# Kernel tuning notes

Hardware: AMD Instinct MI355X
Metric: run time of the kernel (lower is better)

Reference implementation:

```python
import jax, jax.numpy as jnp
import numpy as np

HEADS = 8
DIM_HEAD = 64
MAX_REL = 200  # max_rel_dist


def setup_inputs() -> dict:
    key = jax.random.key(0)
    ks = jax.random.split(key, 5)
    B, N, D = 4, 2048, 512
    x = jax.random.normal(ks[0], (B, N, D), dtype=jnp.float32)
    temporal_mask = jax.random.randint(ks[1], (N, N), 0, 2, dtype=jnp.int32)
    gamma = jnp.ones((D,), jnp.float32)
    beta = jnp.zeros((D,), jnp.float32)
    Wqkv = jax.random.normal(ks[2], (D, 3 * HEADS * DIM_HEAD), dtype=jnp.float32) * 0.02
    Wout = jax.random.normal(ks[3], (HEADS * DIM_HEAD, D), dtype=jnp.float32) * 0.02
    bout = jnp.zeros((D,), jnp.float32)
    rel_table = jax.random.normal(ks[4], (2 * MAX_REL - 1,), dtype=jnp.float32) * 0.02
    return {"x": x, "gamma": gamma, "beta": beta, "Wqkv": Wqkv, "Wout": Wout,
            "bout": bout, "rel_table": rel_table, "temporal_mask": temporal_mask}


def reference(x, gamma, beta, Wqkv, Wout, bout, rel_table, temporal_mask):
    B, N, D = x.shape
    scale = DIM_HEAD ** -0.5
    # LayerNorm
    mu = jnp.mean(x, axis=-1, keepdims=True)
    var = jnp.mean(jnp.square(x - mu), axis=-1, keepdims=True)
    xn = (x - mu) * jax.lax.rsqrt(var + 1e-5) * gamma + beta
    # QKV projection (no bias), split heads: b n (h d) -> b h n d
    qkv = xn @ Wqkv  # [B, N, 3*H*d]
    q, k, v = jnp.split(qkv, 3, axis=-1)
    split = lambda t: t.reshape(B, N, HEADS, DIM_HEAD).transpose(0, 2, 1, 3)
    q, k, v = split(q), split(k), split(v)
    # scores with learned relative-position bias
    dots = jnp.einsum('bhnd,bhmd->bhnm', q, k) * scale  # [B,H,N,N]
    idx = jnp.arange(N)
    rel = jnp.clip(idx[:, None] - idx[None, :], -(MAX_REL - 1), MAX_REL - 1) + MAX_REL - 1
    dots = dots + rel_table[rel][None, None, :, :]
    # temporal mask (0 -> -inf); large negative for grad safety
    dots = jnp.where(temporal_mask[None, None, :, :] == 0, jnp.float32(-1e9), dots)
    attn = jax.nn.softmax(dots, axis=-1)
    out = jnp.einsum('bhnm,bhmd->bhnd', attn, v)
    out = out.transpose(0, 2, 1, 3).reshape(B, N, HEADS * DIM_HEAD)
    return out @ Wout + bout
```

## Files before the change

### kernel.cpp

```cpp
#include <hip/hip_runtime.h>

typedef __attribute__((ext_vector_type(8))) short bf16x8;
typedef __attribute__((ext_vector_type(4))) short bf16x4;
typedef __attribute__((ext_vector_type(4))) float f32x4;
typedef unsigned short ushort_t;

#define B_ 4
#define H_ 8
#define N_ 2048
#define D_ 512
#define MAXREL 199
#define LOG2E 1.4426950408889634f

__device__ __forceinline__ ushort_t f2bf(float f) {
    union { float f; unsigned u; } v; v.f = f;
    unsigned r = v.u + 0x7fffu + ((v.u >> 16) & 1u);
    return (ushort_t)(r >> 16);
}
__device__ __forceinline__ float bf2f(ushort_t u) {
    union { unsigned u; float f; } v; v.u = ((unsigned)u) << 16;
    return v.f;
}
__device__ __forceinline__ float fexp2(float x) {
#if __has_builtin(__builtin_amdgcn_exp2f)
    return __builtin_amdgcn_exp2f(x);
#else
    return __expf(x * 0.6931471805599453f);
#endif
}
__device__ __forceinline__ unsigned cvt_pk_bf16(float lo, float hi) {
    unsigned r;
    asm("v_cvt_pk_bf16_f32 %0, %1, %2" : "=v"(r) : "v"(lo), "v"(hi));
    return r;
}
__device__ __forceinline__ void gl_lds16(const ushort_t* g, ushort_t* l) {
    __builtin_amdgcn_global_load_lds(
        (const __attribute__((address_space(1))) void*)g,
        (__attribute__((address_space(3))) void*)l,
        16, 0, 0);
}

#define PREP_BIAS  16384
#define PREP_LN    8192
#define PREP_WQ    768
#define PREP_WO    256
__global__ __launch_bounds__(256) void prep_kernel(const float* __restrict__ x,
                                                   const float* __restrict__ gamma,
                                                   const float* __restrict__ beta,
                                                   ushort_t* __restrict__ xn,
                                                   const float* __restrict__ Wqkv,
                                                   ushort_t* __restrict__ WqkvT,
                                                   const float* __restrict__ Wout,
                                                   ushort_t* __restrict__ WoutT,
                                                   const float* __restrict__ rel,
                                                   const int* __restrict__ mask,
                                                   ushort_t* __restrict__ bp) {
    __shared__ float smem[32 * 33];
    const int blk = blockIdx.x;
    const int t = threadIdx.x;

    if (blk < PREP_BIAS) {
        int idx = blk * 256 + t;
        int n = idx >> 11, m = idx & 2047;
        int dl = n - m;
        dl = dl < -MAXREL ? -MAXREL : (dl > MAXREL ? MAXREL : dl);
        float v = (mask[idx] == 0) ? -1e9f : rel[dl + MAXREL] * LOG2E;
        int off = ((n >> 7) << 18) + ((m >> 6) << 13) + (((n >> 4) & 7) << 10)
                + (((m >> 4) & 3) << 8) + (((m >> 2) & 3) << 6) + ((n & 15) << 2) + (m & 3);
        bp[off] = f2bf(v);
    } else if (blk < PREP_BIAS + PREP_LN) {
        const int row = blk - PREP_BIAS;
        const float* xr = x + (size_t)row * D_;
        float v0 = xr[t];
        float v1 = xr[t + 256];
        float s = v0 + v1;
        for (int o = 32; o > 0; o >>= 1) s += __shfl_down(s, o);
        if ((t & 63) == 0) smem[t >> 6] = s;
        __syncthreads();
        float mu = (smem[0] + smem[1] + smem[2] + smem[3]) * (1.0f / D_);
        __syncthreads();
        float d0 = v0 - mu, d1 = v1 - mu;
        float s2 = d0 * d0 + d1 * d1;
        for (int o = 32; o > 0; o >>= 1) s2 += __shfl_down(s2, o);
        if ((t & 63) == 0) smem[t >> 6] = s2;
        __syncthreads();
        float var = (smem[0] + smem[1] + smem[2] + smem[3]) * (1.0f / D_);
        float rs = rsqrtf(var + 1e-5f);
        ushort_t* yr = xn + (size_t)row * D_;
        yr[t]       = f2bf(d0 * rs * gamma[t]       + beta[t]);
        yr[t + 256] = f2bf(d1 * rs * gamma[t + 256] + beta[t + 256]);
    } else {
        const float* W; ushort_t* Wt; int Nn, i;
        if (blk < PREP_BIAS + PREP_LN + PREP_WQ) {
            i = blk - (PREP_BIAS + PREP_LN); W = Wqkv; Wt = WqkvT; Nn = 1536;
        } else {
            i = blk - (PREP_BIAS + PREP_LN + PREP_WQ); W = Wout; Wt = WoutT; Nn = 512;
        }
        const int nb = Nn >> 5;
        const int bx = (i % nb) * 32, by = (i / nb) * 32;
        const int tx = t & 31, ty = t >> 5;
        float (*tile)[33] = (float(*)[33])smem;
        #pragma unroll
        for (int k = 0; k < 32; k += 8)
            tile[ty + k][tx] = W[(size_t)(by + ty + k) * Nn + bx + tx];
        __syncthreads();
        #pragma unroll
        for (int k = 0; k < 32; k += 8)
            Wt[(size_t)(bx + ty + k) * 512 + by + tx] = f2bf(tile[tx][ty + k]);
    }
}

__global__ __launch_bounds__(256) void gemm_qkv(const ushort_t* __restrict__ A,
                                                const ushort_t* __restrict__ Bt,
                                                ushort_t* __restrict__ qb,
                                                ushort_t* __restrict__ kb,
                                                ushort_t* __restrict__ vb) {
    __shared__ ushort_t As[128 * 32];
    __shared__ ushort_t Bs[128 * 32];
    const int t = threadIdx.x;
    const int lane = t & 63, w = t >> 6;
    const int m16 = lane & 15, quad = lane >> 4;
    const int wr = w >> 1, wc = w & 1;
    const int r0 = blockIdx.y * 128, c0 = blockIdx.x * 128;

    const ushort_t* Ag = A  + (size_t)(r0 + (t >> 2)) * D_ + (t & 3) * 8;
    const ushort_t* Bg = Bt + (size_t)(c0 + (t >> 2)) * D_ + (t & 3) * 8;
    ushort_t* AsW = As + w * 512;
    ushort_t* BsW = Bs + w * 512;

    f32x4 acc[4][4];
    #pragma unroll
    for (int i = 0; i < 4; i++)
        #pragma unroll
        for (int j = 0; j < 4; j++) acc[i][j] = (f32x4){0.f, 0.f, 0.f, 0.f};

    for (int k0 = 0; k0 < D_; k0 += 32) {
        gl_lds16(Ag + k0, AsW);
        gl_lds16(Ag + k0 + (size_t)64 * D_, AsW + 2048);
        gl_lds16(Bg + k0, BsW);
        gl_lds16(Bg + k0 + (size_t)64 * D_, BsW + 2048);
        __syncthreads();
        bf16x8 af[4], bfr[4];
        #pragma unroll
        for (int rt = 0; rt < 4; rt++)
            af[rt] = *(const bf16x8*)(As + (wr * 64 + rt * 16 + m16) * 32 + quad * 8);
        #pragma unroll
        for (int ct = 0; ct < 4; ct++)
            bfr[ct] = *(const bf16x8*)(Bs + (wc * 64 + ct * 16 + m16) * 32 + quad * 8);
        #pragma unroll
        for (int rt = 0; rt < 4; rt++)
            #pragma unroll
            for (int ct = 0; ct < 4; ct++)
                acc[rt][ct] = __builtin_amdgcn_mfma_f32_16x16x32_bf16(af[rt], bfr[ct], acc[rt][ct], 0, 0, 0);
        __syncthreads();
    }

    #pragma unroll
    for (int ct = 0; ct < 4; ct++) {
        int cc = c0 + wc * 64 + ct * 16;
        int which = cc >> 9;
        int h = (cc >> 6) & 7;
        int d = (cc & 63) + m16;
        #pragma unroll
        for (int rt = 0; rt < 4; rt++) {
            int rowb = r0 + wr * 64 + rt * 16 + quad * 4;
            int b = rowb >> 11, n0 = rowb & 2047;
            if (which == 0) {
                #pragma unroll
                for (int r = 0; r < 4; r++)
                    qb[((size_t)((b * H_ + h) * N_ + n0 + r)) * 64 + d] = f2bf(acc[rt][ct][r] * (0.125f * LOG2E));
            } else if (which == 1) {
                #pragma unroll
                for (int r = 0; r < 4; r++)
                    kb[((size_t)((b * H_ + h) * N_ + n0 + r)) * 64 + d] = f2bf(acc[rt][ct][r]);
            } else {
                union { ushort_t u4[4]; unsigned long long ll; } pk;
                #pragma unroll
                for (int r = 0; r < 4; r++) pk.u4[r] = f2bf(acc[rt][ct][r]);
                *(unsigned long long*)(vb + ((size_t)((b * H_ + h) * 64 + d)) * N_ + n0) = pk.ll;
            }
        }
    }
}

__global__ __launch_bounds__(256) void gemm_out(const ushort_t* __restrict__ A,
                                                const ushort_t* __restrict__ Bt,
                                                const float* __restrict__ bias,
                                                float* __restrict__ C) {
    __shared__ ushort_t As[64 * 32];
    __shared__ ushort_t Bs[128 * 32];
    const int t = threadIdx.x;
    const int lane = t & 63, w = t >> 6;
    const int m16 = lane & 15, quad = lane >> 4;
    const int wr = w >> 1, wc = w & 1;
    const int r0 = blockIdx.y * 64, c0 = blockIdx.x * 128;

    const ushort_t* Ag = A  + (size_t)(r0 + (t >> 2)) * D_ + (t & 3) * 8;
    const ushort_t* Bg = Bt + (size_t)(c0 + (t >> 2)) * D_ + (t & 3) * 8;
    ushort_t* AsW = As + w * 512;
    ushort_t* BsW = Bs + w * 512;

    f32x4 acc[2][4];
    #pragma unroll
    for (int i = 0; i < 2; i++)
        #pragma unroll
        for (int j = 0; j < 4; j++) acc[i][j] = (f32x4){0.f, 0.f, 0.f, 0.f};

    for (int k0 = 0; k0 < D_; k0 += 32) {
        gl_lds16(Ag + k0, AsW);
        gl_lds16(Bg + k0, BsW);
        gl_lds16(Bg + k0 + (size_t)64 * D_, BsW + 2048);
        __syncthreads();
        bf16x8 af[2], bfr[4];
        #pragma unroll
        for (int mf = 0; mf < 2; mf++)
            af[mf] = *(const bf16x8*)(As + (wr * 32 + mf * 16 + m16) * 32 + quad * 8);
        #pragma unroll
        for (int nt = 0; nt < 4; nt++)
            bfr[nt] = *(const bf16x8*)(Bs + (wc * 64 + nt * 16 + m16) * 32 + quad * 8);
        #pragma unroll
        for (int mf = 0; mf < 2; mf++)
            #pragma unroll
            for (int nt = 0; nt < 4; nt++)
                acc[mf][nt] = __builtin_amdgcn_mfma_f32_16x16x32_bf16(af[mf], bfr[nt], acc[mf][nt], 0, 0, 0);
        __syncthreads();
    }

    #pragma unroll
    for (int mf = 0; mf < 2; mf++) {
        #pragma unroll
        for (int nt = 0; nt < 4; nt++) {
            int col = c0 + wc * 64 + nt * 16 + m16;
            int row0 = r0 + wr * 32 + mf * 16 + quad * 4;
            float bv = bias[col];
            #pragma unroll
            for (int r = 0; r < 4; r++)
                C[(size_t)(row0 + r) * 512 + col] = acc[mf][nt][r] + bv;
        }
    }
}

__global__ __launch_bounds__(512, 4) void attn_mfma(const ushort_t* __restrict__ qb,
                                                    const ushort_t* __restrict__ kb,
                                                    const ushort_t* __restrict__ vb,
                                                    const ushort_t* __restrict__ bp,
                                                    ushort_t* __restrict__ attn) {
    __shared__ ushort_t Ks[2][64 * 64];
    __shared__ ushort_t Vs[2][64 * 64];
    __shared__ ushort_t p_s[8][16 * 64];

    const int t = threadIdx.x;
    const int w = t >> 6, lane = t & 63;
    const int m16 = lane & 15, quad = lane >> 4;
    const int id = blockIdx.x;
    const int bh = id & 31;
    const int qt = id >> 5;
    const int b = bh >> 3, h = bh & 7;
    const int n0w = qt * 128 + w * 16;

    const int srow = t >> 3, scb = t & 7;
    const int soff = srow * 64 + (scb ^ (srow & 7)) * 8;
    const ushort_t* kgbase = kb + ((size_t)bh * N_) * 64;
    const ushort_t* vgbase = vb + ((size_t)bh * 64) * N_;

    const ushort_t* qpb = qb + ((size_t)(bh * N_ + n0w + m16)) * 64 + quad * 8;
    bf16x8 qa0 = *(const bf16x8*)(qpb);
    bf16x8 qa1 = *(const bf16x8*)(qpb + 32);

    const ushort_t* bpb = bp + ((size_t)qt << 18) + (w << 10) + (quad << 6) + (m16 << 2);

    *(bf16x8*)(&Ks[0][soff]) = *(const bf16x8*)(kgbase + (size_t)srow * 64 + scb * 8);
    *(bf16x8*)(&Vs[0][soff]) = *(const bf16x8*)(vgbase + (size_t)srow * N_ + scb * 8);
    __syncthreads();

    f32x4 o[4];
    #pragma unroll
    for (int nt = 0; nt < 4; nt++) o[nt] = (f32x4){0.f, 0.f, 0.f, 0.f};
    float rsum = 0.f;

    ushort_t* pw = p_s[w];

    for (int jt = 0; jt < 32; jt++) {
        const int buf = jt & 1;
        const int j0 = jt * 64;
        const bool more = (jt < 31);

        bf16x8 kst, vst;
        if (more) {
            kst = *(const bf16x8*)(kgbase + (size_t)(j0 + 64 + srow) * 64 + scb * 8);
            vst = *(const bf16x8*)(vgbase + (size_t)srow * N_ + j0 + 64 + scb * 8);
        }

        bf16x4 bc[4];
        #pragma unroll
        for (int nt = 0; nt < 4; nt++) bc[nt] = *(const bf16x4*)(bpb + (jt << 13) + (nt << 8));

        unsigned pk[8];
        #pragma unroll
        for (int nt = 0; nt < 4; nt++) {
            f32x4 a2;
            #pragma unroll
            for (int r = 0; r < 4; r++) a2[r] = bf2f((ushort_t)bc[nt][r]);
            int kr = nt * 16 + m16;
            bf16x8 kf0 = *(const bf16x8*)(&Ks[buf][kr * 64 + ((quad) ^ (kr & 7)) * 8]);
            bf16x8 kf1 = *(const bf16x8*)(&Ks[buf][kr * 64 + ((quad + 4) ^ (kr & 7)) * 8]);
            a2 = __builtin_amdgcn_mfma_f32_16x16x32_bf16(kf0, qa0, a2, 0, 0, 0);
            a2 = __builtin_amdgcn_mfma_f32_16x16x32_bf16(kf1, qa1, a2, 0, 0, 0);
            float p0 = fexp2(a2[0]);
            float p1 = fexp2(a2[1]);
            float p2 = fexp2(a2[2]);
            float p3 = fexp2(a2[3]);
            rsum += (p0 + p1) + (p2 + p3);
            pk[nt * 2]     = cvt_pk_bf16(p0, p1);
            pk[nt * 2 + 1] = cvt_pk_bf16(p2, p3);
        }

        #pragma unroll
        for (int j = 0; j < 8; j++) {
            int chunk = 2 * (j >> 1) + (quad >> 1);
            int pos = (quad & 1) * 4 + 2 * (j & 1);
            *(unsigned*)(pw + m16 * 64 + ((chunk ^ (m16 & 7)) << 3) + pos) = pk[j];
        }

        bf16x8 pa0 = *(const bf16x8*)(pw + m16 * 64 + ((quad ^ (m16 & 7)) << 3));
        bf16x8 pa1 = *(const bf16x8*)(pw + m16 * 64 + (((quad + 4) ^ (m16 & 7)) << 3));

        #pragma unroll
        for (int nt = 0; nt < 4; nt++) {
            int d = nt * 16 + m16;
            bf16x8 vf0 = *(const bf16x8*)(&Vs[buf][d * 64 + ((quad) ^ (d & 7)) * 8]);
            bf16x8 vf1 = *(const bf16x8*)(&Vs[buf][d * 64 + ((quad + 4) ^ (d & 7)) * 8]);
            o[nt] = __builtin_amdgcn_mfma_f32_16x16x32_bf16(pa0, vf0, o[nt], 0, 0, 0);
            o[nt] = __builtin_amdgcn_mfma_f32_16x16x32_bf16(pa1, vf1, o[nt], 0, 0, 0);
        }

        if (more) {
            *(bf16x8*)(&Ks[buf ^ 1][soff]) = kst;
            *(bf16x8*)(&Vs[buf ^ 1][soff]) = vst;
        }
        __syncthreads();
    }

    rsum += __shfl_xor(rsum, 16);
    rsum += __shfl_xor(rsum, 32);

    #pragma unroll
    for (int r = 0; r < 4; r++) {
        float inv = 1.0f / __shfl(rsum, quad * 4 + r);
        int n = n0w + quad * 4 + r;
        ushort_t* orow = attn + ((size_t)(b * N_ + n)) * 512 + h * 64 + m16;
        #pragma unroll
        for (int nt = 0; nt < 4; nt++) orow[nt * 16] = f2bf(o[nt][r] * inv);
    }
}

extern "C" void kernel_launch(void* const* d_in, const int* in_sizes, int n_in,
                              void* d_out, int out_size, void* d_ws, size_t ws_size,
                              hipStream_t stream) {
    const float* x     = (const float*)d_in[0];
    const float* gamma = (const float*)d_in[1];
    const float* beta  = (const float*)d_in[2];
    const float* Wqkv  = (const float*)d_in[3];
    const float* Wout  = (const float*)d_in[4];
    const float* bout  = (const float*)d_in[5];
    const float* rel   = (const float*)d_in[6];
    const int*   mask  = (const int*)d_in[7];
    float* out = (float*)d_out;

    char* wsb = (char*)d_ws;
    ushort_t* xn    = (ushort_t*)(wsb);
    ushort_t* attnb = (ushort_t*)(wsb + ( 8u << 20));
    ushort_t* qb    = (ushort_t*)(wsb + (16u << 20));
    ushort_t* kb    = (ushort_t*)(wsb + (24u << 20));
    ushort_t* vb    = (ushort_t*)(wsb + (32u << 20));
    ushort_t* WqkvT = (ushort_t*)(wsb + (40u << 20));
    ushort_t* WoutT = (ushort_t*)(wsb + (42u << 20));
    ushort_t* bp    = (ushort_t*)(wsb + (44u << 20));

    prep_kernel<<<PREP_BIAS + PREP_LN + PREP_WQ + PREP_WO, 256, 0, stream>>>(
        x, gamma, beta, xn, Wqkv, WqkvT, Wout, WoutT, rel, mask, bp);

    gemm_qkv<<<dim3(1536 / 128, 8192 / 128), 256, 0, stream>>>(xn, WqkvT, qb, kb, vb);

    attn_mfma<<<512, 512, 0, stream>>>(qb, kb, vb, bp, attnb);

    gemm_out<<<dim3(512 / 128, 8192 / 64), 256, 0, stream>>>(attnb, WoutT, bout, out);
}
```

Measured before the change: 200.4 us.

## Deepen attention K/V/bias prefetch to two tiles ahead with priority hints

Restructures the attention main loop into a manually unrolled pair of tiles with ping-pong register sets, so K/V global loads are issued two tiles ahead and the bias block one tile ahead. This gives global-load latency more time to hide behind the MFMA and exp work. It also wraps the MFMA sections in s_setprio to favor matrix issue, and merges the P stores to LDS into 64-bit writes. The extra live registers risk spilling or lower occupancy under the 512-thread, 4-block launch bound.

Result: faster. 188.7 us (-5.8%).

```diff
diff --git a/kernel.cpp b/kernel.cpp
--- a/kernel.cpp
+++ b/kernel.cpp
@@ -240,6 +240,65 @@
     }
 }
 
+#define ATTN_TILE(JT, KCUR, VCUR, KNXT, VNXT, BCUR, BNXT)                              \
+  {                                                                                    \
+    const int jt = (JT);                                                               \
+    const int buf = jt & 1;                                                            \
+    if (jt + 2 < 32) {                                                                 \
+      KNXT = *(const bf16x8*)(kgbase + (size_t)((jt + 2) * 64 + srow) * 64 + scb * 8); \
+      VNXT = *(const bf16x8*)(vgbase + (size_t)srow * N_ + (jt + 2) * 64 + scb * 8);   \
+    }                                                                                  \
+    if (jt + 1 < 32) {                                                                 \
+      _Pragma("unroll")                                                                \
+      for (int nt = 0; nt < 4; nt++)                                                   \
+        BNXT[nt] = *(const bf16x4*)(bpb + ((jt + 1) << 13) + (nt << 8));               \
+    }                                                                                  \
+    unsigned pk[8];                                                                    \
+    __builtin_amdgcn_s_setprio(1);                                                     \
+    _Pragma("unroll")                                                                  \
+    for (int nt = 0; nt < 4; nt++) {                                                   \
+      f32x4 a2;                                                                        \
+      _Pragma("unroll")                                                                \
+      for (int r = 0; r < 4; r++) a2[r] = bf2f((ushort_t)BCUR[nt][r]);                 \
+      int kr = nt * 16 + m16;                                                          \
+      bf16x8 kf0 = *(const bf16x8*)(&Ks[buf][kr * 64 + ((quad) ^ (kr & 7)) * 8]);      \
+      bf16x8 kf1 = *(const bf16x8*)(&Ks[buf][kr * 64 + ((quad + 4) ^ (kr & 7)) * 8]);  \
+      a2 = __builtin_amdgcn_mfma_f32_16x16x32_bf16(kf0, qa0, a2, 0, 0, 0);             \
+      a2 = __builtin_amdgcn_mfma_f32_16x16x32_bf16(kf1, qa1, a2, 0, 0, 0);             \
+      float p0 = fexp2(a2[0]), p1 = fexp2(a2[1]);                                      \
+      float p2 = fexp2(a2[2]), p3 = fexp2(a2[3]);                                      \
+      rsum += (p0 + p1) + (p2 + p3);                                                   \
+      pk[nt * 2]     = cvt_pk_bf16(p0, p1);                                            \
+      pk[nt * 2 + 1] = cvt_pk_bf16(p2, p3);                                            \
+    }                                                                                  \
+    __builtin_amdgcn_s_setprio(0);                                                     \
+    _Pragma("unroll")                                                                  \
+    for (int i = 0; i < 4; i++) {                                                      \
+      int chunk = 2 * i + (quad >> 1);                                                 \
+      union { unsigned uu[2]; unsigned long long ll; } wrp;                            \
+      wrp.uu[0] = pk[2 * i]; wrp.uu[1] = pk[2 * i + 1];                                \
+      *(unsigned long long*)(pw + m16 * 64 + ((chunk ^ (m16 & 7)) << 3)                \
+                             + (quad & 1) * 4) = wrp.ll;                               \
+    }                                                                                  \
+    bf16x8 pa0 = *(const bf16x8*)(pw + m16 * 64 + ((quad ^ (m16 & 7)) << 3));          \
+    bf16x8 pa1 = *(const bf16x8*)(pw + m16 * 64 + (((quad + 4) ^ (m16 & 7)) << 3));    \
+    __builtin_amdgcn_s_setprio(1);                                                     \
+    _Pragma("unroll")                                                                  \
+    for (int nt = 0; nt < 4; nt++) {                                                   \
+      int d = nt * 16 + m16;                                                           \
+      bf16x8 vf0 = *(const bf16x8*)(&Vs[buf][d * 64 + ((quad) ^ (d & 7)) * 8]);        \
+      bf16x8 vf1 = *(const bf16x8*)(&Vs[buf][d * 64 + ((quad + 4) ^ (d & 7)) * 8]);    \
+      o[nt] = __builtin_amdgcn_mfma_f32_16x16x32_bf16(pa0, vf0, o[nt], 0, 0, 0);       \
+      o[nt] = __builtin_amdgcn_mfma_f32_16x16x32_bf16(pa1, vf1, o[nt], 0, 0, 0);       \
+    }                                                                                  \
+    __builtin_amdgcn_s_setprio(0);                                                     \
+    if (jt + 1 < 32) {                                                                 \
+      *(bf16x8*)(&Ks[buf ^ 1][soff]) = KCUR;                                           \
+      *(bf16x8*)(&Vs[buf ^ 1][soff]) = VCUR;                                           \
+    }                                                                                  \
+    __syncthreads();                                                                   \
+  }
+
 __global__ __launch_bounds__(512, 4) void attn_mfma(const ushort_t* __restrict__ qb,
                                                     const ushort_t* __restrict__ kb,
                                                     const ushort_t* __restrict__ vb,
@@ -271,6 +330,12 @@
 
     *(bf16x8*)(&Ks[0][soff]) = *(const bf16x8*)(kgbase + (size_t)srow * 64 + scb * 8);
     *(bf16x8*)(&Vs[0][soff]) = *(const bf16x8*)(vgbase + (size_t)srow * N_ + scb * 8);
+    bf16x8 kA = *(const bf16x8*)(kgbase + (size_t)(64 + srow) * 64 + scb * 8);
+    bf16x8 vA = *(const bf16x8*)(vgbase + (size_t)srow * N_ + 64 + scb * 8);
+    bf16x8 kB, vB;
+    bf16x4 bA[4], bB[4];
+    #pragma unroll
+    for (int nt = 0; nt < 4; nt++) bA[nt] = *(const bf16x4*)(bpb + (nt << 8));
     __syncthreads();
 
     f32x4 o[4];
@@ -280,65 +345,9 @@
 
     ushort_t* pw = p_s[w];
 
-    for (int jt = 0; jt < 32; jt++) {
-        const int buf = jt & 1;
-        const int j0 = jt * 64;
-        const bool more = (jt < 31);
-
-        bf16x8 kst, vst;
-        if (more) {
-            kst = *(const bf16x8*)(kgbase + (size_t)(j0 + 64 + srow) * 64 + scb * 8);
-            vst = *(const bf16x8*)(vgbase + (size_t)srow * N_ + j0 + 64 + scb * 8);
-        }
-
-        bf16x4 bc[4];
-        #pragma unroll
-        for (int nt = 0; nt < 4; nt++) bc[nt] = *(const bf16x4*)(bpb + (jt << 13) + (nt << 8));
-
-        unsigned pk[8];
-        #pragma unroll
-        for (int nt = 0; nt < 4; nt++) {
-            f32x4 a2;
-            #pragma unroll
-            for (int r = 0; r < 4; r++) a2[r] = bf2f((ushort_t)bc[nt][r]);
-            int kr = nt * 16 + m16;
-            bf16x8 kf0 = *(const bf16x8*)(&Ks[buf][kr * 64 + ((quad) ^ (kr & 7)) * 8]);
-            bf16x8 kf1 = *(const bf16x8*)(&Ks[buf][kr * 64 + ((quad + 4) ^ (kr & 7)) * 8]);
-            a2 = __builtin_amdgcn_mfma_f32_16x16x32_bf16(kf0, qa0, a2, 0, 0, 0);
-            a2 = __builtin_amdgcn_mfma_f32_16x16x32_bf16(kf1, qa1, a2, 0, 0, 0);
-            float p0 = fexp2(a2[0]);
-            float p1 = fexp2(a2[1]);
-            float p2 = fexp2(a2[2]);
-            float p3 = fexp2(a2[3]);
-            rsum += (p0 + p1) + (p2 + p3);
-            pk[nt * 2]     = cvt_pk_bf16(p0, p1);
-            pk[nt * 2 + 1] = cvt_pk_bf16(p2, p3);
-        }
-
-        #pragma unroll
-        for (int j = 0; j < 8; j++) {
-            int chunk = 2 * (j >> 1) + (quad >> 1);
-            int pos = (quad & 1) * 4 + 2 * (j & 1);
-            *(unsigned*)(pw + m16 * 64 + ((chunk ^ (m16 & 7)) << 3) + pos) = pk[j];
-        }
-
-        bf16x8 pa0 = *(const bf16x8*)(pw + m16 * 64 + ((quad ^ (m16 & 7)) << 3));
-        bf16x8 pa1 = *(const bf16x8*)(pw + m16 * 64 + (((quad + 4) ^ (m16 & 7)) << 3));
-
-        #pragma unroll
-        for (int nt = 0; nt < 4; nt++) {
-            int d = nt * 16 + m16;
-            bf16x8 vf0 = *(const bf16x8*)(&Vs[buf][d * 64 + ((quad) ^ (d & 7)) * 8]);
-            bf16x8 vf1 = *(const bf16x8*)(&Vs[buf][d * 64 + ((quad + 4) ^ (d & 7)) * 8]);
-            o[nt] = __builtin_amdgcn_mfma_f32_16x16x32_bf16(pa0, vf0, o[nt], 0, 0, 0);
-            o[nt] = __builtin_amdgcn_mfma_f32_16x16x32_bf16(pa1, vf1, o[nt], 0, 0, 0);
-        }
-
-        if (more) {
-            *(bf16x8*)(&Ks[buf ^ 1][soff]) = kst;
-            *(bf16x8*)(&Vs[buf ^ 1][soff]) = vst;
-        }
-        __syncthreads();
+    for (int jt2 = 0; jt2 < 16; jt2++) {
+        ATTN_TILE(2 * jt2,     kA, vA, kB, vB, bA, bB);
+        ATTN_TILE(2 * jt2 + 1, kB, vB, kA, vA, bB, bA);
     }
 
     rsum += __shfl_xor(rsum, 16);
```
